# Optimization experiments

Hardware: AMD Instinct MI355X
Metric: run time of the kernel (lower is better)

Reference implementation:

```python
import jax, jax.numpy as jnp
import numpy as np

B, D = 262144, 256  # D even; halves are D//2 = 128
H = 256             # MLP hidden width


def setup_inputs() -> dict:
    key = jax.random.key(0)
    k_x, k_w1, k_w2 = jax.random.split(key, 3)
    M = D // 2
    x = jax.random.normal(k_x, (B, D), dtype=jnp.float32)
    W1 = jax.random.normal(k_w1, (M, H), dtype=jnp.float32) * (1.0 / np.sqrt(M))
    b1 = jnp.zeros((H,), dtype=jnp.float32)
    W2 = jax.random.normal(k_w2, (H, M), dtype=jnp.float32) * (1.0 / np.sqrt(H))
    b2 = jnp.zeros((M,), dtype=jnp.float32)
    return {"x": x, "W1": W1, "b1": b1, "W2": W2, "b2": b2}


def reference(x, W1, b1, W2, b2):
    # partition == 'even': first = even columns, second = odd columns
    first = x[:, 0::2]   # [B, D//2]
    second = x[:, 1::2]  # [B, D//2]
    # non_linear_model m(first): 2-layer MLP with ReLU
    m = jax.nn.relu(first @ W1 + b1) @ W2 + b2  # [B, D//2]
    # additive coupling law (NICE): a + b
    coupled = second + m
    # _interleave(first, coupled, 'even'): out[:,0::2]=first, out[:,1::2]=coupled
    out = jnp.stack([first, coupled], axis=-1).reshape(x.shape[0], -1)  # [B, D]
    return out
```

## Files before the change

### kernel.cpp

```cpp
#include <hip/hip_runtime.h>

typedef __attribute__((ext_vector_type(8))) short bf16x8;
typedef __attribute__((ext_vector_type(4))) float f32x4;

__device__ __forceinline__ unsigned short f2bf(float f) {
    union { float f; unsigned int u; } v; v.f = f;
    unsigned int r = v.u + 0x7fffu + ((v.u >> 16) & 1u);
    return (unsigned short)(r >> 16);
}
__device__ __forceinline__ float bf2f(unsigned short h) {
    union { unsigned int u; float f; } v; v.u = ((unsigned int)h) << 16;
    return v.f;
}

__global__ void prep_weights(const float* __restrict__ W1, const float* __restrict__ W2,
                             unsigned short* __restrict__ wbuf) {
    int t = blockIdx.x * 256 + threadIdx.x;
    int j = t & 7, l = (t >> 3) & 63, f = (t >> 9) & 63;
    float v;
    if (t < 32768) {
        int kk = f >> 4, nn = f & 15;
        int k = kk * 32 + ((l >> 4) << 3) + j;
        int n = nn * 16 + (l & 15);
        v = W1[k * 256 + n];
    } else {
        int kk = f >> 3, nn = f & 7;
        int k = kk * 32 + ((l >> 4) << 3) + j;
        int n = nn * 16 + (l & 15);
        v = W2[k * 128 + n];
    }
    wbuf[t] = f2bf(v);
}

__global__ __launch_bounds__(256, 2)
void coupling_main(const float* __restrict__ x, const unsigned short* __restrict__ wbuf,
                   const float* __restrict__ b1, const float* __restrict__ b2,
                   float* __restrict__ out) {
    __shared__ unsigned short sFirst[64 * 128];
    __shared__ unsigned short sSecond[64 * 128];
    __shared__ unsigned short sH[64 * 256];

    const int tid = threadIdx.x;
    const int lane = tid & 63;
    const int w = tid >> 6;
    const int l15 = lane & 15;
    const int grp = lane >> 4;
    const int row0 = blockIdx.x * 64;

    bf16x8 w1f[4][4];
#pragma unroll
    for (int kk = 0; kk < 4; ++kk)
#pragma unroll
      for (int ni = 0; ni < 4; ++ni) {
        int f = kk * 16 + (4 * w + ni);
        w1f[kk][ni] = *reinterpret_cast<const bf16x8*>(wbuf + (f * 64 + lane) * 8);
      }
    float b1v[4];
#pragma unroll
    for (int ni = 0; ni < 4; ++ni) b1v[ni] = b1[w * 64 + ni * 16 + l15];

    const float4* xt = reinterpret_cast<const float4*>(x + (size_t)row0 * 256);
#pragma unroll
    for (int i = 0; i < 16; ++i) {
        int f4 = i * 256 + tid;
        float4 v = xt[f4];
        int row = f4 >> 6, c4 = f4 & 63;
        unsigned int fp = (unsigned int)f2bf(v.x) | ((unsigned int)f2bf(v.z) << 16);
        unsigned int sp = (unsigned int)f2bf(v.y) | ((unsigned int)f2bf(v.w) << 16);
        int slot = (c4 >> 2) ^ (row & 15);
        reinterpret_cast<unsigned int*>(sFirst)[row * 64 + slot * 4 + (c4 & 3)] = fp;
        reinterpret_cast<unsigned int*>(sSecond)[row * 64 + slot * 4 + (c4 & 3)] = sp;
    }
    __syncthreads();

    f32x4 hacc[4][4];
#pragma unroll
    for (int mi = 0; mi < 4; ++mi)
#pragma unroll
      for (int ni = 0; ni < 4; ++ni)
        hacc[mi][ni] = (f32x4){0.f, 0.f, 0.f, 0.f};

#pragma unroll
    for (int mi = 0; mi < 4; ++mi) {
        int row = mi * 16 + l15;
        bf16x8 a[4];
#pragma unroll
        for (int kk = 0; kk < 4; ++kk) {
            int slot = (kk * 4 + grp) ^ (row & 15);
            a[kk] = *reinterpret_cast<const bf16x8*>(sFirst + row * 128 + slot * 8);
        }
#pragma unroll
        for (int kk = 0; kk < 4; ++kk)
#pragma unroll
          for (int ni = 0; ni < 4; ++ni)
            hacc[mi][ni] = __builtin_amdgcn_mfma_f32_16x16x32_bf16(a[kk], w1f[kk][ni], hacc[mi][ni], 0, 0, 0);
    }

    bf16x8 w2f[8][2];
#pragma unroll
    for (int kk = 0; kk < 8; ++kk)
#pragma unroll
      for (int ni = 0; ni < 2; ++ni) {
        int f = kk * 8 + (2 * w + ni);
        w2f[kk][ni] = *reinterpret_cast<const bf16x8*>(wbuf + 32768 + (f * 64 + lane) * 8);
      }
    float b2v[2];
#pragma unroll
    for (int ni = 0; ni < 2; ++ni) b2v[ni] = b2[w * 32 + ni * 16 + l15];

#pragma unroll
    for (int mi = 0; mi < 4; ++mi)
#pragma unroll
      for (int ni = 0; ni < 4; ++ni) {
        int col = w * 64 + ni * 16 + l15;
#pragma unroll
        for (int r = 0; r < 4; ++r) {
            int row = mi * 16 + grp * 4 + r;
            float hv = hacc[mi][ni][r] + b1v[ni];
            hv = fmaxf(hv, 0.f);
            int slot = (col >> 3) ^ (row & 15);
            sH[row * 256 + slot * 8 + (col & 7)] = f2bf(hv);
        }
      }
    __syncthreads();

    f32x4 macc[4][2];
#pragma unroll
    for (int mi = 0; mi < 4; ++mi)
#pragma unroll
      for (int ni = 0; ni < 2; ++ni)
        macc[mi][ni] = (f32x4){0.f, 0.f, 0.f, 0.f};

#pragma unroll
    for (int mi = 0; mi < 4; ++mi) {
        int row = mi * 16 + l15;
        bf16x8 a[8];
#pragma unroll
        for (int kk = 0; kk < 8; ++kk) {
            int slot = (kk * 4 + grp) ^ (row & 15);
            a[kk] = *reinterpret_cast<const bf16x8*>(sH + row * 256 + slot * 8);
        }
#pragma unroll
        for (int kk = 0; kk < 8; ++kk)
#pragma unroll
          for (int ni = 0; ni < 2; ++ni)
            macc[mi][ni] = __builtin_amdgcn_mfma_f32_16x16x32_bf16(a[kk], w2f[kk][ni], macc[mi][ni], 0, 0, 0);
    }

#pragma unroll
    for (int mi = 0; mi < 4; ++mi)
#pragma unroll
      for (int ni = 0; ni < 2; ++ni) {
        int col = w * 32 + ni * 16 + l15;
#pragma unroll
        for (int r = 0; r < 4; ++r) {
            int row = mi * 16 + grp * 4 + r;
            int slotF = (col >> 3) ^ (row & 15);
            float fv = bf2f(sFirst[row * 128 + slotF * 8 + (col & 7)]);
            float sv = bf2f(sSecond[row * 128 + slotF * 8 + (col & 7)]);
            float mv = macc[mi][ni][r] + b2v[ni];
            float2 o = make_float2(fv, sv + mv);
            *reinterpret_cast<float2*>(out + (size_t)(row0 + row) * 256 + col * 2) = o;
        }
      }
}

extern "C" void kernel_launch(void* const* d_in, const int* in_sizes, int n_in,
                              void* d_out, int out_size, void* d_ws, size_t ws_size,
                              hipStream_t stream) {
    const float* x  = (const float*)d_in[0];
    const float* W1 = (const float*)d_in[1];
    const float* b1 = (const float*)d_in[2];
    const float* W2 = (const float*)d_in[3];
    const float* b2 = (const float*)d_in[4];
    float* out = (float*)d_out;
    unsigned short* wbuf = (unsigned short*)d_ws;

    int Brows = in_sizes[0] / 256;
    prep_weights<<<256, 256, 0, stream>>>(W1, W2, wbuf);
    coupling_main<<<Brows / 64, 256, 0, stream>>>(x, wbuf, b1, b2, out);
}
```

Measured before the change: 115.9 us.

## Keep odd columns in registers, drop sSecond, stream weights per k-step

Each thread now loads its own (even, odd) float2 pairs from x in the same layout it later writes. The odd value stays in fp32 registers and the sSecond shared buffer is removed. Weight fragments are loaded per k-step rather than held in registers for the whole kernel, and launch bounds rise to 3 blocks per CU. This cuts LDS use and register pressure to allow more occupancy and keeps the second half in full precision, at the cost of less coalesced float2 global loads and repeated weight loads inside the MFMA loops.

```diff
diff --git a/kernel.cpp b/kernel.cpp
--- a/kernel.cpp
+++ b/kernel.cpp
@@ -32,12 +32,11 @@
     wbuf[t] = f2bf(v);
 }
 
-__global__ __launch_bounds__(256, 2)
+__global__ __launch_bounds__(256, 3)
 void coupling_main(const float* __restrict__ x, const unsigned short* __restrict__ wbuf,
                    const float* __restrict__ b1, const float* __restrict__ b2,
                    float* __restrict__ out) {
     __shared__ unsigned short sFirst[64 * 128];
-    __shared__ unsigned short sSecond[64 * 128];
     __shared__ unsigned short sH[64 * 256];
 
     const int tid = threadIdx.x;
@@ -47,30 +46,22 @@
     const int grp = lane >> 4;
     const int row0 = blockIdx.x * 64;
 
-    bf16x8 w1f[4][4];
+    float sec[4][2][4];
 #pragma unroll
-    for (int kk = 0; kk < 4; ++kk)
+    for (int mi = 0; mi < 4; ++mi)
 #pragma unroll
-      for (int ni = 0; ni < 4; ++ni) {
-        int f = kk * 16 + (4 * w + ni);
-        w1f[kk][ni] = *reinterpret_cast<const bf16x8*>(wbuf + (f * 64 + lane) * 8);
+      for (int ni = 0; ni < 2; ++ni) {
+        int col = w * 32 + ni * 16 + l15;
+#pragma unroll
+        for (int r = 0; r < 4; ++r) {
+            int row = mi * 16 + grp * 4 + r;
+            const float2 fs = *reinterpret_cast<const float2*>(
+                x + (size_t)(row0 + row) * 256 + col * 2);
+            sec[mi][ni][r] = fs.y;
+            int slot = (col >> 3) ^ (row & 15);
+            sFirst[row * 128 + slot * 8 + (col & 7)] = f2bf(fs.x);
+        }
       }
-    float b1v[4];
-#pragma unroll
-    for (int ni = 0; ni < 4; ++ni) b1v[ni] = b1[w * 64 + ni * 16 + l15];
-
-    const float4* xt = reinterpret_cast<const float4*>(x + (size_t)row0 * 256);
-#pragma unroll
-    for (int i = 0; i < 16; ++i) {
-        int f4 = i * 256 + tid;
-        float4 v = xt[f4];
-        int row = f4 >> 6, c4 = f4 & 63;
-        unsigned int fp = (unsigned int)f2bf(v.x) | ((unsigned int)f2bf(v.z) << 16);
-        unsigned int sp = (unsigned int)f2bf(v.y) | ((unsigned int)f2bf(v.w) << 16);
-        int slot = (c4 >> 2) ^ (row & 15);
-        reinterpret_cast<unsigned int*>(sFirst)[row * 64 + slot * 4 + (c4 & 3)] = fp;
-        reinterpret_cast<unsigned int*>(sSecond)[row * 64 + slot * 4 + (c4 & 3)] = sp;
-    }
     __syncthreads();
 
     f32x4 hacc[4][4];
@@ -81,32 +72,26 @@
         hacc[mi][ni] = (f32x4){0.f, 0.f, 0.f, 0.f};
 
 #pragma unroll
-    for (int mi = 0; mi < 4; ++mi) {
-        int row = mi * 16 + l15;
-        bf16x8 a[4];
+    for (int kk = 0; kk < 4; ++kk) {
+        bf16x8 w1k[4];
 #pragma unroll
-        for (int kk = 0; kk < 4; ++kk) {
-            int slot = (kk * 4 + grp) ^ (row & 15);
-            a[kk] = *reinterpret_cast<const bf16x8*>(sFirst + row * 128 + slot * 8);
+        for (int ni = 0; ni < 4; ++ni)
+            w1k[ni] = *reinterpret_cast<const bf16x8*>(
+                wbuf + ((kk * 16 + 4 * w + ni) * 64 + lane) * 8);
+#pragma unroll
+        for (int mi = 0; mi < 4; ++mi) {
+            int row = mi * 16 + l15;
+            int slot = (kk * 4 + grp) ^ l15;
+            bf16x8 a = *reinterpret_cast<const bf16x8*>(sFirst + row * 128 + slot * 8);
+#pragma unroll
+            for (int ni = 0; ni < 4; ++ni)
+                hacc[mi][ni] = __builtin_amdgcn_mfma_f32_16x16x32_bf16(a, w1k[ni], hacc[mi][ni], 0, 0, 0);
         }
-#pragma unroll
-        for (int kk = 0; kk < 4; ++kk)
-#pragma unroll
-          for (int ni = 0; ni < 4; ++ni)
-            hacc[mi][ni] = __builtin_amdgcn_mfma_f32_16x16x32_bf16(a[kk], w1f[kk][ni], hacc[mi][ni], 0, 0, 0);
     }
 
-    bf16x8 w2f[8][2];
+    float b1v[4];
 #pragma unroll
-    for (int kk = 0; kk < 8; ++kk)
-#pragma unroll
-      for (int ni = 0; ni < 2; ++ni) {
-        int f = kk * 8 + (2 * w + ni);
-        w2f[kk][ni] = *reinterpret_cast<const bf16x8*>(wbuf + 32768 + (f * 64 + lane) * 8);
-      }
-    float b2v[2];
-#pragma unroll
-    for (int ni = 0; ni < 2; ++ni) b2v[ni] = b2[w * 32 + ni * 16 + l15];
+    for (int ni = 0; ni < 4; ++ni) b1v[ni] = b1[w * 64 + ni * 16 + l15];
 
 #pragma unroll
     for (int mi = 0; mi < 4; ++mi)
@@ -124,6 +109,10 @@
       }
     __syncthreads();
 
+    float b2v[2];
+#pragma unroll
+    for (int ni = 0; ni < 2; ++ni) b2v[ni] = b2[w * 32 + ni * 16 + l15];
+
     f32x4 macc[4][2];
 #pragma unroll
     for (int mi = 0; mi < 4; ++mi)
@@ -132,19 +121,21 @@
         macc[mi][ni] = (f32x4){0.f, 0.f, 0.f, 0.f};
 
 #pragma unroll
-    for (int mi = 0; mi < 4; ++mi) {
-        int row = mi * 16 + l15;
-        bf16x8 a[8];
+    for (int kk = 0; kk < 8; ++kk) {
+        bf16x8 w2k[2];
 #pragma unroll
-        for (int kk = 0; kk < 8; ++kk) {
-            int slot = (kk * 4 + grp) ^ (row & 15);
-            a[kk] = *reinterpret_cast<const bf16x8*>(sH + row * 256 + slot * 8);
+        for (int ni = 0; ni < 2; ++ni)
+            w2k[ni] = *reinterpret_cast<const bf16x8*>(
+                wbuf + 32768 + ((kk * 8 + 2 * w + ni) * 64 + lane) * 8);
+#pragma unroll
+        for (int mi = 0; mi < 4; ++mi) {
+            int row = mi * 16 + l15;
+            int slot = (kk * 4 + grp) ^ l15;
+            bf16x8 a = *reinterpret_cast<const bf16x8*>(sH + row * 256 + slot * 8);
+#pragma unroll
+            for (int ni = 0; ni < 2; ++ni)
+                macc[mi][ni] = __builtin_amdgcn_mfma_f32_16x16x32_bf16(a, w2k[ni], macc[mi][ni], 0, 0, 0);
         }
-#pragma unroll
-        for (int kk = 0; kk < 8; ++kk)
-#pragma unroll
-          for (int ni = 0; ni < 2; ++ni)
-            macc[mi][ni] = __builtin_amdgcn_mfma_f32_16x16x32_bf16(a[kk], w2f[kk][ni], macc[mi][ni], 0, 0, 0);
     }
 
 #pragma unroll
@@ -157,9 +148,8 @@
             int row = mi * 16 + grp * 4 + r;
             int slotF = (col >> 3) ^ (row & 15);
             float fv = bf2f(sFirst[row * 128 + slotF * 8 + (col & 7)]);
-            float sv = bf2f(sSecond[row * 128 + slotF * 8 + (col & 7)]);
             float mv = macc[mi][ni][r] + b2v[ni];
-            float2 o = make_float2(fv, sv + mv);
+            float2 o = make_float2(fv, sec[mi][ni][r] + mv);
             *reinterpret_cast<float2*>(out + (size_t)(row0 + row) * 256 + col * 2) = o;
         }
       }
```

Result: slower. 323.8 us (+179.4%).
